# Optimization experiments

Measured on AMD Instinct MI355X. Metric: run time of the kernel, lower is better.

## Reference

```python
import jax, jax.numpy as jnp
import numpy as np

B, C, H, W = 32, 256, 32, 32
HID, NPATH = 128, 4


def setup_inputs() -> dict:
    key = jax.random.key(0)
    ks = jax.random.split(key, 16)
    s = lambda *sh: 1.0 / np.sqrt(sh[-1])
    inp = {
        "lidar": jax.random.normal(ks[0], (B, C, H, W), jnp.float32),
        "hsi": jax.random.normal(ks[1], (B, C, H, W), jnp.float32),
        "x": jax.random.normal(ks[2], (B, C, H, W), jnp.float32),
        # shared Cross_Self_attention params
        "Wq": jax.random.normal(ks[3], (C, C), jnp.float32) * s(C, C),
        "bq": jnp.zeros((C,), jnp.float32),
        "Wk": jax.random.normal(ks[4], (C, C), jnp.float32) * s(C, C),
        "bk": jnp.zeros((C,), jnp.float32),
        "Wv": jax.random.normal(ks[5], (C, C), jnp.float32) * s(C, C),
        "bv": jnp.zeros((C,), jnp.float32),
        # 1x1 conv: [out=C, in=2C]
        "conv_w": jax.random.normal(ks[6], (C, 2 * C), jnp.float32) * s(C, 2 * C),
        "conv_b": jnp.zeros((C,), jnp.float32),
        # router MLP
        "r_w1": jax.random.normal(ks[7], (HID, 2 * C), jnp.float32) * s(HID, 2 * C),
        "r_b1": jnp.zeros((HID,), jnp.float32),
        "r_w2": jax.random.normal(ks[8], (NPATH, HID), jnp.float32) * s(NPATH, HID),
        "r_b2": jnp.zeros((NPATH,), jnp.float32),
    }
    return inp


def _cross_self_attn(xq, yv, Wq, bq, Wk, bk, Wv, bv):
    # xq, yv: [b, s, c]
    q = xq @ Wq.T + bq
    k = xq @ Wk.T + bk
    v = yv @ Wv.T + bv
    probs = jax.nn.softmax(jnp.einsum("bsc,btc->bst", q, k), axis=-1)  # [b,s,s]
    return jnp.einsum("bst,btc->bsc", probs, q * v)  # bilinear value Q*V


def reference(lidar, hsi, x, Wq, bq, Wk, bk, Wv, bv, conv_w, conv_b, r_w1, r_b1, r_w2, r_b2):
    b, c, h, w = lidar.shape
    # Router: concat channels, spatial mean pool, MLP, sigmoid
    g = jnp.concatenate([lidar, hsi], axis=1).mean(axis=(2, 3))  # [b, 2c]
    path_prob = jax.nn.sigmoid(jax.nn.relu(g @ r_w1.T + r_b1) @ r_w2.T + r_b2)

    l = lidar.reshape(b, c, h * w).transpose(0, 2, 1)  # b (h w) c
    hh = hsi.reshape(b, c, h * w).transpose(0, 2, 1)

    h_emb = _cross_self_attn(l, hh, Wq, bq, Wk, bk, Wv, bv)  # [b, hw, c]
    l_emb = _cross_self_attn(hh, l, Wq, bq, Wk, bk, Wv, bv)

    h_emb = h_emb.transpose(0, 2, 1).reshape(b, c, h, w)
    l_emb = l_emb.transpose(0, 2, 1).reshape(b, c, h, w)

    cat = jnp.concatenate([l_emb, h_emb], axis=1)  # [b, 2c, h, w]
    emb = jnp.einsum("bihw,oi->bohw", cat, conv_w) + conv_b[None, :, None, None] + x
    return emb, path_prob
```

## Files before the change

### kernel.cpp

```cpp
#include <hip/hip_runtime.h>
#include <stdint.h>

typedef unsigned short u16;
typedef unsigned int u32;
typedef _Float16 f16;
typedef _Float16 f16x8 __attribute__((ext_vector_type(8)));
typedef _Float16 f16x4 __attribute__((ext_vector_type(4)));
typedef float f32x4 __attribute__((ext_vector_type(4)));

#define B_ 32
#define C_ 256
#define S_ 1024

__global__ __launch_bounds__(256) void k_mlp(
    const float* __restrict__ g,
    const float* __restrict__ w1, const float* __restrict__ b1,
    const float* __restrict__ w2, const float* __restrict__ b2,
    float* __restrict__ out)
{
    int b = blockIdx.x, tid = threadIdx.x;
    __shared__ float sg[512];
    __shared__ float sh[128];
    sg[tid]     = g[b*512 + tid]       * (1.0f/1024.0f);
    sg[tid+256] = g[b*512 + 256 + tid] * (1.0f/1024.0f);
    __syncthreads();
    if (tid < 128){
        float a = b1[tid];
        const float* w = w1 + (size_t)tid*512;
        #pragma unroll 4
        for (int k = 0; k < 512; k += 4){
            float4 wv = *(const float4*)(w + k);
            a += sg[k]*wv.x + sg[k+1]*wv.y + sg[k+2]*wv.z + sg[k+3]*wv.w;
        }
        sh[tid] = fmaxf(a, 0.f);
    }
    __syncthreads();
    if (tid < 4){
        float a = b2[tid];
        const float* w = w2 + (size_t)tid*128;
        for (int k = 0; k < 128; ++k) a += sh[k]*w[k];
        out[(size_t)8388608 + b*4 + tid] = 1.f/(1.f+expf(-a));
    }
}

__global__ __launch_bounds__(256) void k_cvtw(
    const float* __restrict__ Wq, const float* __restrict__ Wk,
    const float* __restrict__ Wv, const float* __restrict__ cw,
    f16* __restrict__ Wqf, f16* __restrict__ Wkf,
    f16* __restrict__ Wvf, f16* __restrict__ cwf)
{
    int i = (blockIdx.x*256 + threadIdx.x) * 4;
    const float* src; f16* dst; int off;
    if (i < 65536){ src = Wq; dst = Wqf; off = i; }
    else if (i < 131072){ src = Wk; dst = Wkf; off = i - 65536; }
    else if (i < 196608){ src = Wv; dst = Wvf; off = i - 131072; }
    else { src = cw; dst = cwf; off = i - 196608; }
    float4 v = *(const float4*)(src + off);
    f16x4 r = { (f16)v.x, (f16)v.y, (f16)v.z, (f16)v.w };
    *(f16x4*)(dst + off) = r;
}

__global__ __launch_bounds__(256) void k_cvt(
    const float* __restrict__ lidar, const float* __restrict__ hsi,
    f16* __restrict__ lidT, f16* __restrict__ hsiT,
    float* __restrict__ g)
{
    int z = blockIdx.z, which = z >> 5, b = z & 31;
    const float* src = (which ? hsi : lidar) + (size_t)b*C_*S_;
    f16* dst = (which ? hsiT : lidT) + (size_t)b*S_*C_;
    int tid = threadIdx.x;
    int c4 = blockIdx.y*64 + (tid&15)*4;
    int s4 = blockIdx.x*64 + (tid>>4)*4;
    float4 m[4];
    #pragma unroll
    for (int r = 0; r < 4; ++r) m[r] = *(const float4*)(src + (size_t)(c4+r)*S_ + s4);
    f16x4 t0 = { (f16)m[0].x, (f16)m[1].x, (f16)m[2].x, (f16)m[3].x };
    f16x4 t1 = { (f16)m[0].y, (f16)m[1].y, (f16)m[2].y, (f16)m[3].y };
    f16x4 t2 = { (f16)m[0].z, (f16)m[1].z, (f16)m[2].z, (f16)m[3].z };
    f16x4 t3 = { (f16)m[0].w, (f16)m[1].w, (f16)m[2].w, (f16)m[3].w };
    *(f16x4*)(dst + (size_t)(s4+0)*C_ + c4) = t0;
    *(f16x4*)(dst + (size_t)(s4+1)*C_ + c4) = t1;
    *(f16x4*)(dst + (size_t)(s4+2)*C_ + c4) = t2;
    *(f16x4*)(dst + (size_t)(s4+3)*C_ + c4) = t3;
    float ps[4];
    #pragma unroll
    for (int r = 0; r < 4; ++r){
        ps[r] = m[r].x + m[r].y + m[r].z + m[r].w;
        ps[r] += __shfl_xor(ps[r], 16, 64);
        ps[r] += __shfl_xor(ps[r], 32, 64);
    }
    __shared__ float sred[4][64];
    int wv = tid>>6, lane = tid&63;
    if ((lane>>4) == 0){
        #pragma unroll
        for (int r = 0; r < 4; ++r) sred[wv][(lane&15)*4 + r] = ps[r];
    }
    __syncthreads();
    if (tid < 64){
        float v = sred[0][tid] + sred[1][tid] + sred[2][tid] + sred[3][tid];
        atomicAdd(&g[b*512 + which*256 + blockIdx.y*64 + tid], v);
    }
}

__global__ __launch_bounds__(256) void k_qkv(
    const f16* __restrict__ lidT, const f16* __restrict__ hsiT,
    const f16* __restrict__ Wqf, const f16* __restrict__ Wkf, const f16* __restrict__ Wvf,
    const float* __restrict__ bq, const float* __restrict__ bk, const float* __restrict__ bv,
    f16* __restrict__ Qf_l, f16* __restrict__ Kf_l,
    f16* __restrict__ Qf_h, f16* __restrict__ Kf_h,
    f16* __restrict__ Qt_l, f16* __restrict__ Qt_h,
    f16* __restrict__ Vt_l, f16* __restrict__ Vt_h)
{
    int z = blockIdx.z, combo = z >> 5, b = z & 31, ww = combo % 3;
    const f16* In = ((combo < 3) ? lidT : hsiT) + (size_t)b*S_*C_;
    const f16* Wf = (ww==0) ? Wqf : (ww==1) ? Wkf : Wvf;
    const float* bias = (ww==0) ? bq : (ww==1) ? bk : bv;
    int s0 = blockIdx.x*64, o0 = blockIdx.y*64;
    int tid = threadIdx.x, w = tid>>6, lane = tid&63, quad = lane>>4, l15 = lane&15;

    __shared__ __align__(16) f16 sA[64*72];
    __shared__ __align__(16) f16 sB[64*72];

    f32x4 D[4];
    #pragma unroll
    for (int i = 0; i < 4; ++i) D[i] = (f32x4){0.f,0.f,0.f,0.f};

    int row = tid>>2, c16 = (tid&3)*16;
    for (int c0 = 0; c0 < 256; c0 += 64){
        __syncthreads();
        *(f16x8*)&sA[row*72 + c16]     = *(const f16x8*)(In + (size_t)(s0+row)*C_ + c0 + c16);
        *(f16x8*)&sA[row*72 + c16 + 8] = *(const f16x8*)(In + (size_t)(s0+row)*C_ + c0 + c16 + 8);
        *(f16x8*)&sB[row*72 + c16]     = *(const f16x8*)(Wf + (size_t)(o0+row)*C_ + c0 + c16);
        *(f16x8*)&sB[row*72 + c16 + 8] = *(const f16x8*)(Wf + (size_t)(o0+row)*C_ + c0 + c16 + 8);
        __syncthreads();
        #pragma unroll
        for (int sub = 0; sub < 2; ++sub){
            f16x8 a = *(const f16x8*)&sA[(w*16+l15)*72 + sub*32 + quad*8];
            #pragma unroll
            for (int bt = 0; bt < 4; ++bt){
                f16x8 bb = *(const f16x8*)&sB[(bt*16+l15)*72 + sub*32 + quad*8];
                D[bt] = __builtin_amdgcn_mfma_f32_16x16x32_f16(a, bb, D[bt], 0,0,0);
            }
        }
    }
    float bi[4];
    #pragma unroll
    for (int bt = 0; bt < 4; ++bt) bi[bt] = bias[o0 + bt*16 + l15];

    if (ww == 0){
        f16* F = ((combo==0) ? Qf_l : Qf_h) + (size_t)b*S_*C_;
        #pragma unroll
        for (int bt = 0; bt < 4; ++bt)
            #pragma unroll
            for (int r = 0; r < 4; ++r)
                F[(size_t)(s0 + w*16 + quad*4 + r)*C_ + o0 + bt*16 + l15] = (f16)(D[bt][r] + bi[bt]);
    } else if (ww == 1){
        f16* F = ((combo==1) ? Kf_l : Kf_h) + (size_t)b*S_*C_;
        #pragma unroll
        for (int bt = 0; bt < 4; ++bt)
            #pragma unroll
            for (int r = 0; r < 4; ++r)
                F[(size_t)(s0 + w*16 + quad*4 + r)*C_ + o0 + bt*16 + l15] = (f16)(D[bt][r] + bi[bt]);
    }
    if (ww != 1){
        __syncthreads();
        #pragma unroll
        for (int bt = 0; bt < 4; ++bt)
            #pragma unroll
            for (int r = 0; r < 4; ++r)
                sA[(bt*16+l15)*72 + w*16 + quad*4 + r] = (f16)(D[bt][r] + bi[bt]);
        __syncthreads();
        f16* T = (combo==0) ? Qt_l : (combo==3) ? Qt_h : (combo==2) ? Vt_l : Vt_h;
        T += (size_t)b*C_*S_;
        int o_r = tid>>2, s16b = (tid&3)*16;
        *(f16x8*)(T + (size_t)(o0+o_r)*S_ + s0 + s16b)     = *(const f16x8*)&sA[o_r*72 + s16b];
        *(f16x8*)(T + (size_t)(o0+o_r)*S_ + s0 + s16b + 8) = *(const f16x8*)&sA[o_r*72 + s16b + 8];
    }
}

__global__ __launch_bounds__(256) void k_qv(
    const f16* __restrict__ Qt_l, const f16* __restrict__ Qt_h,
    const f16* __restrict__ Vt_l, const f16* __restrict__ Vt_h,
    f16* __restrict__ QVT1, f16* __restrict__ QVT2)
{
    size_t idx = (size_t)(blockIdx.x*256 + threadIdx.x) * 8;
    f16x8 a = *(const f16x8*)(Qt_l+idx);
    f16x8 b = *(const f16x8*)(Vt_h+idx);
    *(f16x8*)(QVT1+idx) = a*b;
    f16x8 c = *(const f16x8*)(Qt_h+idx);
    f16x8 d = *(const f16x8*)(Vt_l+idx);
    *(f16x8*)(QVT2+idx) = c*d;
}

__global__ __launch_bounds__(256, 2) void k_attn(
    const f16* __restrict__ Qf_l, const f16* __restrict__ Kf_l,
    const f16* __restrict__ Qf_h, const f16* __restrict__ Kf_h,
    const f16* __restrict__ QVT1, const f16* __restrict__ QVT2,
    f16* __restrict__ cat)
{
    int inst = blockIdx.y;
    int b = inst >> 1, which = inst & 1;
    const f16* Qf  = (which ? Qf_h : Qf_l) + (size_t)b*S_*C_;
    const f16* Kf  = (which ? Kf_h : Kf_l) + (size_t)b*S_*C_;
    const f16* QVT = (which ? QVT2 : QVT1) + (size_t)b*C_*S_;
    f16* outp = cat + (size_t)b*S_*512 + (which ? 0 : 256);
    int s0 = blockIdx.x*64;
    int tid = threadIdx.x, w = tid>>6, lane = tid&63, quad = lane>>4, l15 = lane&15;

    __shared__ __align__(16) f16 sK[64*264];
    __shared__ __align__(16) f16 sV[256*72];
    __shared__ __align__(16) f16 sPw[4][16*66];

    f16x8 qa[8];
    {
        const f16* qrow = Qf + (size_t)(s0 + w*16 + l15)*C_ + quad*8;
        #pragma unroll
        for (int i = 0; i < 8; ++i) qa[i] = *(const f16x8*)(qrow + i*32);
    }
    float mrun[4], lrun[4];
    #pragma unroll
    for (int r = 0; r < 4; ++r){ mrun[r] = -1e30f; lrun[r] = 0.f; }
    f32x4 pacc[16];
    #pragma unroll
    for (int i = 0; i < 16; ++i) pacc[i] = (f32x4){0.f,0.f,0.f,0.f};

    for (int tt = 0; tt < 16; ++tt){
        int t0 = tt*64;
        __syncthreads();
        #pragma unroll
        for (int p = 0; p < 8; ++p){
            int idx = p*256 + tid;
            int row = idx >> 5, c8 = (idx & 31)*8;
            *(f16x8*)&sK[row*264 + c8] = *(const f16x8*)(Kf + (size_t)(t0+row)*C_ + c8);
        }
        #pragma unroll
        for (int p = 0; p < 8; ++p){
            int idx = p*256 + tid;
            int row = idx >> 3, t8 = (idx & 7)*8;
            *(f16x8*)&sV[row*72 + t8] = *(const f16x8*)(QVT + (size_t)row*S_ + t0 + t8);
        }
        __syncthreads();

        f32x4 sacc[4];
        #pragma unroll
        for (int bt = 0; bt < 4; ++bt) sacc[bt] = (f32x4){0.f,0.f,0.f,0.f};
        #pragma unroll
        for (int ks = 0; ks < 8; ++ks){
            #pragma unroll
            for (int bt = 0; bt < 4; ++bt){
                f16x8 kb = *(const f16x8*)&sK[(bt*16+l15)*264 + ks*32 + quad*8];
                sacc[bt] = __builtin_amdgcn_mfma_f32_16x16x32_f16(qa[ks], kb, sacc[bt], 0,0,0);
            }
        }

        float alpha[4], lsum[4];
        #pragma unroll
        for (int r = 0; r < 4; ++r){
            float tm = fmaxf(fmaxf(sacc[0][r], sacc[1][r]), fmaxf(sacc[2][r], sacc[3][r]));
            #pragma unroll
            for (int off = 1; off < 16; off <<= 1) tm = fmaxf(tm, __shfl_xor(tm, off, 64));
            float mn = fmaxf(mrun[r], tm);
            alpha[r] = __expf(mrun[r] - mn);
            mrun[r] = mn;
            float acc = 0.f;
            #pragma unroll
            for (int bt = 0; bt < 4; ++bt){
                float p = __expf(sacc[bt][r] - mn);
                sPw[w][(quad*4+r)*66 + bt*16 + l15] = (f16)p;
                acc += p;
            }
            #pragma unroll
            for (int off = 1; off < 16; off <<= 1) acc += __shfl_xor(acc, off, 64);
            lsum[r] = acc;
            lrun[r] = lrun[r]*alpha[r] + lsum[r];
        }
        #pragma unroll
        for (int cf = 0; cf < 16; ++cf)
            #pragma unroll
            for (int r = 0; r < 4; ++r) pacc[cf][r] *= alpha[r];

        f16x8 pa0 = *(const f16x8*)&sPw[w][l15*66 + quad*8];
        f16x8 pa1 = *(const f16x8*)&sPw[w][l15*66 + 32 + quad*8];

        #pragma unroll
        for (int cf = 0; cf < 16; ++cf){
            f16x8 vb0 = *(const f16x8*)&sV[(cf*16+l15)*72 + quad*8];
            f16x8 vb1 = *(const f16x8*)&sV[(cf*16+l15)*72 + 32 + quad*8];
            pacc[cf] = __builtin_amdgcn_mfma_f32_16x16x32_f16(pa0, vb0, pacc[cf], 0,0,0);
            pacc[cf] = __builtin_amdgcn_mfma_f32_16x16x32_f16(pa1, vb1, pacc[cf], 0,0,0);
        }
    }

    #pragma unroll
    for (int r = 0; r < 4; ++r){
        int s = w*16 + quad*4 + r;
        float rl = 1.f / lrun[r];
        #pragma unroll
        for (int cf = 0; cf < 16; ++cf)
            outp[(size_t)(s0+s)*512 + cf*16 + l15] = (f16)(pacc[cf][r] * rl);
    }
}

__global__ __launch_bounds__(256) void k_conv(
    const f16* __restrict__ cat, const f16* __restrict__ cwf,
    const float* __restrict__ cb, const float* __restrict__ x,
    float* __restrict__ out)
{
    int b = blockIdx.z;
    int s0 = blockIdx.x*64, o0 = blockIdx.y*64;
    int tid = threadIdx.x, w = tid>>6, lane = tid&63, quad = lane>>4, l15 = lane&15;

    __shared__ __align__(16) f16 sA[64*72];
    __shared__ __align__(16) f16 sB[64*72];

    f32x4 D[4];
    #pragma unroll
    for (int i = 0; i < 4; ++i) D[i] = (f32x4){0.f,0.f,0.f,0.f};

    const f16* catb = cat + (size_t)b*S_*512;
    int row = tid>>2, c16 = (tid&3)*16;
    for (int i0 = 0; i0 < 512; i0 += 64){
        __syncthreads();
        *(f16x8*)&sA[row*72 + c16]     = *(const f16x8*)(cwf + (size_t)(o0+row)*512 + i0 + c16);
        *(f16x8*)&sA[row*72 + c16 + 8] = *(const f16x8*)(cwf + (size_t)(o0+row)*512 + i0 + c16 + 8);
        *(f16x8*)&sB[row*72 + c16]     = *(const f16x8*)(catb + (size_t)(s0+row)*512 + i0 + c16);
        *(f16x8*)&sB[row*72 + c16 + 8] = *(const f16x8*)(catb + (size_t)(s0+row)*512 + i0 + c16 + 8);
        __syncthreads();
        #pragma unroll
        for (int sub = 0; sub < 2; ++sub){
            f16x8 a = *(const f16x8*)&sA[(w*16+l15)*72 + sub*32 + quad*8];
            #pragma unroll
            for (int bt = 0; bt < 4; ++bt){
                f16x8 bb = *(const f16x8*)&sB[(bt*16+l15)*72 + sub*32 + quad*8];
                D[bt] = __builtin_amdgcn_mfma_f32_16x16x32_f16(a, bb, D[bt], 0,0,0);
            }
        }
    }
    #pragma unroll
    for (int r = 0; r < 4; ++r){
        int o_loc = w*16 + quad*4 + r;
        float cbv = cb[o0 + o_loc];
        size_t base = (size_t)b*C_*S_ + (size_t)(o0+o_loc)*S_ + s0;
        #pragma unroll
        for (int bt = 0; bt < 4; ++bt){
            size_t a = base + bt*16 + l15;
            out[a] = D[bt][r] + cbv + x[a];
        }
    }
}

extern "C" void kernel_launch(void* const* d_in, const int* in_sizes, int n_in,
                              void* d_out, int out_size, void* d_ws, size_t ws_size,
                              hipStream_t stream)
{
    const float* lidar = (const float*)d_in[0];
    const float* hsi   = (const float*)d_in[1];
    const float* x     = (const float*)d_in[2];
    const float* Wq = (const float*)d_in[3];  const float* bq = (const float*)d_in[4];
    const float* Wk = (const float*)d_in[5];  const float* bk = (const float*)d_in[6];
    const float* Wv = (const float*)d_in[7];  const float* bv = (const float*)d_in[8];
    const float* cw = (const float*)d_in[9];  const float* cb = (const float*)d_in[10];
    const float* rw1 = (const float*)d_in[11]; const float* rb1 = (const float*)d_in[12];
    const float* rw2 = (const float*)d_in[13]; const float* rb2 = (const float*)d_in[14];
    float* outF = (float*)d_out;
    char* ws = (char*)d_ws;
    const size_t M = 1ull<<20;

    f16* lidT = (f16*)(ws +   0*M);
    f16* hsiT = (f16*)(ws +  16*M);
    f16* Qf_l = (f16*)(ws +  32*M);
    f16* Kf_l = (f16*)(ws +  48*M);
    f16* Qf_h = (f16*)(ws +  64*M);
    f16* Kf_h = (f16*)(ws +  80*M);
    f16* Qt_l = (f16*)(ws +  96*M);
    f16* Qt_h = (f16*)(ws + 112*M);
    f16* cat  = (f16*)(ws + 128*M);
    float* g  = (float*)(ws + 160*M);
    f16* Wqf  = (f16*)(ws + 161*M);
    f16* Wkf  = (f16*)(ws + 161*M + 131072);
    f16* Wvf  = (f16*)(ws + 161*M + 262144);
    f16* cwf  = (f16*)(ws + 161*M + 393216);
    f16* QVT1 = lidT;
    f16* QVT2 = hsiT;
    f16* Vt_l = (f16*)d_out;
    f16* Vt_h = (f16*)d_out + 8388608;

    hipMemsetAsync(g, 0, 4096*sizeof(float), stream);
    k_cvtw<<<320, 256, 0, stream>>>(Wq, Wk, Wv, cw, Wqf, Wkf, Wvf, cwf);
    k_cvt<<<dim3(16,4,64), 256, 0, stream>>>(lidar, hsi, lidT, hsiT, g);
    k_mlp<<<32, 256, 0, stream>>>(g, rw1, rb1, rw2, rb2, outF);
    k_qkv<<<dim3(16,4,192), 256, 0, stream>>>(lidT, hsiT, Wqf, Wkf, Wvf, bq, bk, bv,
                                              Qf_l, Kf_l, Qf_h, Kf_h, Qt_l, Qt_h, Vt_l, Vt_h);
    k_qv<<<4096, 256, 0, stream>>>(Qt_l, Qt_h, Vt_l, Vt_h, QVT1, QVT2);
    k_attn<<<dim3(16,64), 256, 0, stream>>>(Qf_l, Kf_l, Qf_h, Kf_h, QVT1, QVT2, cat);
    k_conv<<<dim3(16,4,32), 256, 0, stream>>>(cat, cwf, cb, x, outF);
}
```

Measured before the change: 412.7 us.

## Fuse Q*V product into attention kernel, share LDS buffer, lazy softmax rescale

Removes the separate k_qv kernel and computes the Q*V elementwise product while staging the value tile into shared memory. K and V tiles now share one LDS buffer loaded in sequence, which cuts shared memory so three blocks fit per CU. The online softmax skips rescaling unless the running max grows by more than a threshold, and the row-sum shuffle reduction moves to the end. MFMA sections get raised wave priority. The trade-offs are an extra barrier per tile and reading two value tensors per tile, Q and V, where one precomputed product was read before. That means more global traffic inside the attention loop.

```diff
diff --git a/kernel.cpp b/kernel.cpp
--- a/kernel.cpp
+++ b/kernel.cpp
@@ -178,37 +178,24 @@
     }
 }
 
-__global__ __launch_bounds__(256) void k_qv(
+__global__ __launch_bounds__(256, 3) void k_attn(
+    const f16* __restrict__ Qf_l, const f16* __restrict__ Kf_l,
+    const f16* __restrict__ Qf_h, const f16* __restrict__ Kf_h,
     const f16* __restrict__ Qt_l, const f16* __restrict__ Qt_h,
     const f16* __restrict__ Vt_l, const f16* __restrict__ Vt_h,
-    f16* __restrict__ QVT1, f16* __restrict__ QVT2)
-{
-    size_t idx = (size_t)(blockIdx.x*256 + threadIdx.x) * 8;
-    f16x8 a = *(const f16x8*)(Qt_l+idx);
-    f16x8 b = *(const f16x8*)(Vt_h+idx);
-    *(f16x8*)(QVT1+idx) = a*b;
-    f16x8 c = *(const f16x8*)(Qt_h+idx);
-    f16x8 d = *(const f16x8*)(Vt_l+idx);
-    *(f16x8*)(QVT2+idx) = c*d;
-}
-
-__global__ __launch_bounds__(256, 2) void k_attn(
-    const f16* __restrict__ Qf_l, const f16* __restrict__ Kf_l,
-    const f16* __restrict__ Qf_h, const f16* __restrict__ Kf_h,
-    const f16* __restrict__ QVT1, const f16* __restrict__ QVT2,
     f16* __restrict__ cat)
 {
     int inst = blockIdx.y;
     int b = inst >> 1, which = inst & 1;
     const f16* Qf  = (which ? Qf_h : Qf_l) + (size_t)b*S_*C_;
     const f16* Kf  = (which ? Kf_h : Kf_l) + (size_t)b*S_*C_;
-    const f16* QVT = (which ? QVT2 : QVT1) + (size_t)b*C_*S_;
+    const f16* Qt  = (which ? Qt_h : Qt_l) + (size_t)b*C_*S_;
+    const f16* Vt  = (which ? Vt_l : Vt_h) + (size_t)b*C_*S_;
     f16* outp = cat + (size_t)b*S_*512 + (which ? 0 : 256);
     int s0 = blockIdx.x*64;
     int tid = threadIdx.x, w = tid>>6, lane = tid&63, quad = lane>>4, l15 = lane&15;
 
-    __shared__ __align__(16) f16 sK[64*264];
-    __shared__ __align__(16) f16 sV[256*72];
+    __shared__ __align__(16) f16 sBuf[256*72];
     __shared__ __align__(16) f16 sPw[4][16*66];
 
     f16x8 qa[8];
@@ -217,9 +204,9 @@
         #pragma unroll
         for (int i = 0; i < 8; ++i) qa[i] = *(const f16x8*)(qrow + i*32);
     }
-    float mrun[4], lrun[4];
-    #pragma unroll
-    for (int r = 0; r < 4; ++r){ mrun[r] = -1e30f; lrun[r] = 0.f; }
+    float mrun[4], lpart[4];
+    #pragma unroll
+    for (int r = 0; r < 4; ++r){ mrun[r] = -1e30f; lpart[r] = 0.f; }
     f32x4 pacc[16];
     #pragma unroll
     for (int i = 0; i < 16; ++i) pacc[i] = (f32x4){0.f,0.f,0.f,0.f};
@@ -231,70 +218,90 @@
         for (int p = 0; p < 8; ++p){
             int idx = p*256 + tid;
             int row = idx >> 5, c8 = (idx & 31)*8;
-            *(f16x8*)&sK[row*264 + c8] = *(const f16x8*)(Kf + (size_t)(t0+row)*C_ + c8);
-        }
+            *(f16x8*)&sBuf[row*264 + c8] = *(const f16x8*)(Kf + (size_t)(t0+row)*C_ + c8);
+        }
+        __syncthreads();
+
+        f32x4 sacc[4];
+        #pragma unroll
+        for (int bt = 0; bt < 4; ++bt) sacc[bt] = (f32x4){0.f,0.f,0.f,0.f};
+        __builtin_amdgcn_s_setprio(1);
+        #pragma unroll
+        for (int ks = 0; ks < 8; ++ks){
+            #pragma unroll
+            for (int bt = 0; bt < 4; ++bt){
+                f16x8 kb = *(const f16x8*)&sBuf[(bt*16+l15)*264 + ks*32 + quad*8];
+                sacc[bt] = __builtin_amdgcn_mfma_f32_16x16x32_f16(qa[ks], kb, sacc[bt], 0,0,0);
+            }
+        }
+        __builtin_amdgcn_s_setprio(0);
+
+        float tm[4];
+        #pragma unroll
+        for (int r = 0; r < 4; ++r){
+            float t = fmaxf(fmaxf(sacc[0][r], sacc[1][r]), fmaxf(sacc[2][r], sacc[3][r]));
+            #pragma unroll
+            for (int off = 1; off < 16; off <<= 1) t = fmaxf(t, __shfl_xor(t, off, 64));
+            tm[r] = t;
+        }
+        bool need = (tm[0] > mrun[0]+8.f) | (tm[1] > mrun[1]+8.f) |
+                    (tm[2] > mrun[2]+8.f) | (tm[3] > mrun[3]+8.f);
+        if (__any(need)){
+            #pragma unroll
+            for (int r = 0; r < 4; ++r){
+                float mn = fmaxf(mrun[r], tm[r]);
+                float al = __expf(mrun[r] - mn);
+                mrun[r] = mn;
+                lpart[r] *= al;
+                #pragma unroll
+                for (int cf = 0; cf < 16; ++cf) pacc[cf][r] *= al;
+            }
+        }
+        #pragma unroll
+        for (int r = 0; r < 4; ++r){
+            float local = 0.f;
+            #pragma unroll
+            for (int bt = 0; bt < 4; ++bt){
+                float p = __expf(sacc[bt][r] - mrun[r]);
+                sPw[w][(quad*4+r)*66 + bt*16 + l15] = (f16)p;
+                local += p;
+            }
+            lpart[r] += local;
+        }
+        f16x8 pa0 = *(const f16x8*)&sPw[w][l15*66 + quad*8];
+        f16x8 pa1 = *(const f16x8*)&sPw[w][l15*66 + 32 + quad*8];
+
+        __syncthreads();
         #pragma unroll
         for (int p = 0; p < 8; ++p){
             int idx = p*256 + tid;
             int row = idx >> 3, t8 = (idx & 7)*8;
-            *(f16x8*)&sV[row*72 + t8] = *(const f16x8*)(QVT + (size_t)row*S_ + t0 + t8);
-        }
-        __syncthreads();
-
-        f32x4 sacc[4];
-        #pragma unroll
-        for (int bt = 0; bt < 4; ++bt) sacc[bt] = (f32x4){0.f,0.f,0.f,0.f};
-        #pragma unroll
-        for (int ks = 0; ks < 8; ++ks){
-            #pragma unroll
-            for (int bt = 0; bt < 4; ++bt){
-                f16x8 kb = *(const f16x8*)&sK[(bt*16+l15)*264 + ks*32 + quad*8];
-                sacc[bt] = __builtin_amdgcn_mfma_f32_16x16x32_f16(qa[ks], kb, sacc[bt], 0,0,0);
-            }
-        }
-
-        float alpha[4], lsum[4];
-        #pragma unroll
-        for (int r = 0; r < 4; ++r){
-            float tm = fmaxf(fmaxf(sacc[0][r], sacc[1][r]), fmaxf(sacc[2][r], sacc[3][r]));
-            #pragma unroll
-            for (int off = 1; off < 16; off <<= 1) tm = fmaxf(tm, __shfl_xor(tm, off, 64));
-            float mn = fmaxf(mrun[r], tm);
-            alpha[r] = __expf(mrun[r] - mn);
-            mrun[r] = mn;
-            float acc = 0.f;
-            #pragma unroll
-            for (int bt = 0; bt < 4; ++bt){
-                float p = __expf(sacc[bt][r] - mn);
-                sPw[w][(quad*4+r)*66 + bt*16 + l15] = (f16)p;
-                acc += p;
-            }
-            #pragma unroll
-            for (int off = 1; off < 16; off <<= 1) acc += __shfl_xor(acc, off, 64);
-            lsum[r] = acc;
-            lrun[r] = lrun[r]*alpha[r] + lsum[r];
-        }
-        #pragma unroll
-        for (int cf = 0; cf < 16; ++cf)
-            #pragma unroll
-            for (int r = 0; r < 4; ++r) pacc[cf][r] *= alpha[r];
-
-        f16x8 pa0 = *(const f16x8*)&sPw[w][l15*66 + quad*8];
-        f16x8 pa1 = *(const f16x8*)&sPw[w][l15*66 + 32 + quad*8];
-
+            f16x8 a = *(const f16x8*)(Qt + (size_t)row*S_ + t0 + t8);
+            f16x8 v = *(const f16x8*)(Vt + (size_t)row*S_ + t0 + t8);
+            *(f16x8*)&sBuf[row*72 + t8] = a*v;
+        }
+        __syncthreads();
+
+        __builtin_amdgcn_s_setprio(1);
         #pragma unroll
         for (int cf = 0; cf < 16; ++cf){
-            f16x8 vb0 = *(const f16x8*)&sV[(cf*16+l15)*72 + quad*8];
-            f16x8 vb1 = *(const f16x8*)&sV[(cf*16+l15)*72 + 32 + quad*8];
+            f16x8 vb0 = *(const f16x8*)&sBuf[(cf*16+l15)*72 + quad*8];
+            f16x8 vb1 = *(const f16x8*)&sBuf[(cf*16+l15)*72 + 32 + quad*8];
             pacc[cf] = __builtin_amdgcn_mfma_f32_16x16x32_f16(pa0, vb0, pacc[cf], 0,0,0);
             pacc[cf] = __builtin_amdgcn_mfma_f32_16x16x32_f16(pa1, vb1, pacc[cf], 0,0,0);
         }
-    }
-
+        __builtin_amdgcn_s_setprio(0);
+    }
+
+    #pragma unroll
+    for (int r = 0; r < 4; ++r){
+        #pragma unroll
+        for (int off = 1; off < 16; off <<= 1) lpart[r] += __shfl_xor(lpart[r], off, 64);
+    }
     #pragma unroll
     for (int r = 0; r < 4; ++r){
         int s = w*16 + quad*4 + r;
-        float rl = 1.f / lrun[r];
+        float rl = 1.f / lpart[r];
         #pragma unroll
         for (int cf = 0; cf < 16; ++cf)
             outp[(size_t)(s0+s)*512 + cf*16 + l15] = (f16)(pacc[cf][r] * rl);
@@ -380,8 +387,6 @@
     f16* Wkf  = (f16*)(ws + 161*M + 131072);
     f16* Wvf  = (f16*)(ws + 161*M + 262144);
     f16* cwf  = (f16*)(ws + 161*M + 393216);
-    f16* QVT1 = lidT;
-    f16* QVT2 = hsiT;
     f16* Vt_l = (f16*)d_out;
     f16* Vt_h = (f16*)d_out + 8388608;
 
@@ -391,7 +396,6 @@
     k_mlp<<<32, 256, 0, stream>>>(g, rw1, rb1, rw2, rb2, outF);
     k_qkv<<<dim3(16,4,192), 256, 0, stream>>>(lidT, hsiT, Wqf, Wkf, Wvf, bq, bk, bv,
                                               Qf_l, Kf_l, Qf_h, Kf_h, Qt_l, Qt_h, Vt_l, Vt_h);
-    k_qv<<<4096, 256, 0, stream>>>(Qt_l, Qt_h, Vt_l, Vt_h, QVT1, QVT2);
-    k_attn<<<dim3(16,64), 256, 0, stream>>>(Qf_l, Kf_l, Qf_h, Kf_h, QVT1, QVT2, cat);
+    k_attn<<<dim3(16,64), 256, 0, stream>>>(Qf_l, Kf_l, Qf_h, Kf_h, Qt_l, Qt_h, Vt_l, Vt_h, cat);
     k_conv<<<dim3(16,4,32), 256, 0, stream>>>(cat, cwf, cb, x, outF);
 }
```

After: 648.7 us. 1.57x slower.
